# Kernel optimization log

Measured on AMD Instinct MI355X. Metric: run time of the kernel, lower is better.

The kernel has to match this reference:

```python
import jax, jax.numpy as jnp
import numpy as np

N = 40000      # nodes
E = 640000     # directed edges (avg degree 16)
IN_DIM = 64
HID = 64
OUT = 128
EPS_LN = 1e-5
EPS_BN = 1e-5
NEG_SLOPE = 0.2  # PyG GATConv default


def setup_inputs() -> dict:
    key = jax.random.key(0)
    ks = jax.random.split(key, 40)
    s = 0.05
    d = {}
    d["x"] = jax.random.normal(ks[0], (N, IN_DIM), jnp.float32)
    d["edge_index"] = jax.random.randint(ks[1], (2, E), 0, N, jnp.int32)
    d["pos"] = jax.random.normal(ks[2], (N, 3), jnp.float32)
    # GAT layer 1: in=64, out=64, heads=4 (concat)
    d["W1"] = jax.random.normal(ks[3], (4 * HID, IN_DIM), jnp.float32) * s
    d["a_s1"] = jax.random.normal(ks[4], (4, HID), jnp.float32) * s
    d["a_d1"] = jax.random.normal(ks[5], (4, HID), jnp.float32) * s
    d["bg1"] = jnp.zeros((4 * HID,), jnp.float32)
    d["ln1_g"] = jnp.ones((4 * HID,), jnp.float32)
    d["ln1_b"] = jnp.zeros((4 * HID,), jnp.float32)
    # GAT layer 2: in=256, out=64, heads=2 (concat)
    d["W2"] = jax.random.normal(ks[6], (2 * HID, 4 * HID), jnp.float32) * s
    d["a_s2"] = jax.random.normal(ks[7], (2, HID), jnp.float32) * s
    d["a_d2"] = jax.random.normal(ks[8], (2, HID), jnp.float32) * s
    d["bg2"] = jnp.zeros((2 * HID,), jnp.float32)
    d["ln2_g"] = jnp.ones((2 * HID,), jnp.float32)
    d["ln2_b"] = jnp.zeros((2 * HID,), jnp.float32)
    # GAT layer 3: in=128, out=128, heads=1
    d["W3"] = jax.random.normal(ks[9], (OUT, 2 * HID), jnp.float32) * s
    d["a_s3"] = jax.random.normal(ks[10], (1, OUT), jnp.float32) * s
    d["a_d3"] = jax.random.normal(ks[11], (1, OUT), jnp.float32) * s
    d["bg3"] = jnp.zeros((OUT,), jnp.float32)
    # pointnet: Conv1d(3,64,1) -> BN -> ReLU -> Conv1d(64,128,1) -> BN -> ReLU -> Conv1d(128,128,1)
    d["pw1"] = jax.random.normal(ks[12], (64, 3), jnp.float32) * s
    d["pb1"] = jnp.zeros((64,), jnp.float32)
    d["bn1_g"] = jnp.ones((64,), jnp.float32)
    d["bn1_b"] = jnp.zeros((64,), jnp.float32)
    d["pw2"] = jax.random.normal(ks[13], (128, 64), jnp.float32) * s
    d["pb2"] = jnp.zeros((128,), jnp.float32)
    d["bn2_g"] = jnp.ones((128,), jnp.float32)
    d["bn2_b"] = jnp.zeros((128,), jnp.float32)
    d["pw3"] = jax.random.normal(ks[14], (OUT, 128), jnp.float32) * s
    d["pb3"] = jnp.zeros((OUT,), jnp.float32)
    # fusion Linear(2*OUT, OUT)
    d["fw"] = jax.random.normal(ks[15], (OUT, 2 * OUT), jnp.float32) * s
    d["fb"] = jnp.zeros((OUT,), jnp.float32)
    return d


def _gat(x, W, a_s, a_d, b, src, dst, n):
    """PyG-style GATConv (concat=True, eval mode). x:[n,Fin], W:[H*C,Fin], a_*:[H,C]."""
    H, C = a_s.shape
    h = (x @ W.T).reshape(n, H, C)                       # [n,H,C]
    e_src = jnp.sum(h * a_s[None], -1)                   # [n,H]
    e_dst = jnp.sum(h * a_d[None], -1)                   # [n,H]
    e = jax.nn.leaky_relu(e_src[src] + e_dst[dst], NEG_SLOPE)   # [E,H]
    emax = jax.ops.segment_max(e, dst, num_segments=n)   # segment softmax over dst
    ex = jnp.exp(e - emax[dst])
    den = jax.ops.segment_sum(ex, dst, num_segments=n)
    alpha = ex / (den[dst] + 1e-16)                      # [E,H]
    out = jax.ops.segment_sum(alpha[:, :, None] * h[src], dst, num_segments=n)  # [n,H,C]
    return out.reshape(n, H * C) + b


def _ln(x, g, b):
    mu = jnp.mean(x, -1, keepdims=True)
    var = jnp.var(x, -1, keepdims=True)
    return (x - mu) * jax.lax.rsqrt(var + EPS_LN) * g + b


def _bn_eval(x, g, b):
    # eval-mode BatchNorm with freshly-initialized running stats (mean=0, var=1)
    return x * (g * jax.lax.rsqrt(jnp.float32(1.0 + EPS_BN))) + b


def reference(x, edge_index, pos, W1, a_s1, a_d1, bg1, ln1_g, ln1_b,
              W2, a_s2, a_d2, bg2, ln2_g, ln2_b, W3, a_s3, a_d3, bg3,
              pw1, pb1, bn1_g, bn1_b, pw2, pb2, bn2_g, bn2_b, pw3, pb3, fw, fb):
    n = x.shape[0]
    loops = jnp.arange(n, dtype=edge_index.dtype)        # PyG add_self_loops=True
    src = jnp.concatenate([edge_index[0], loops])
    dst = jnp.concatenate([edge_index[1], loops])

    x1 = jax.nn.relu(_ln(_gat(x, W1, a_s1, a_d1, bg1, src, dst, n), ln1_g, ln1_b))
    x2 = jax.nn.relu(_ln(_gat(x1, W2, a_s2, a_d2, bg2, src, dst, n), ln2_g, ln2_b))
    x3 = _gat(x2, W3, a_s3, a_d3, bg3, src, dst, n)      # [n,OUT]

    # pointnet: 1x1 conv1d == per-node linear
    p = jax.nn.relu(_bn_eval(pos @ pw1.T + pb1, bn1_g, bn1_b))
    p = jax.nn.relu(_bn_eval(p @ pw2.T + pb2, bn2_g, bn2_b))
    pos_features = p @ pw3.T + pb3                       # [n,OUT]

    combined = jnp.concatenate([x3, pos_features], -1)
    output = combined @ fw.T + fb
    return (output, x3, pos_features)
```

## Files before the change

### kernel.cpp

```cpp
#include <hip/hip_runtime.h>
#include <cstddef>

#define NNODES 40000
#define NEDGES 640000
#define NETOT  (NNODES + NEDGES)
#define ELLW   96
#define NCAST  30720
#define NBUCK  313
#define SEGCAP 8192
#define ABLOCKS 84
#define CBLOCKS 30
#define GBLK   625

typedef unsigned short u16;
typedef unsigned int   u32;
using v2f = __attribute__((ext_vector_type(2))) float;

__device__ inline float wave_sum(float v) {
#pragma unroll
    for (int o = 32; o > 0; o >>= 1) v += __shfl_xor(v, o);
    return v;
}
__device__ inline u16 f2bf(float f) {
    u32 u = __float_as_uint(f);
    return (u16)((u + 0x7fffu + ((u >> 16) & 1u)) >> 16);
}

__global__ void build_a_kernel(const int* __restrict__ ei, u32* __restrict__ bcnt,
                               u32* __restrict__ seg,
                               const float* __restrict__ W1, const float* __restrict__ as1,
                               const float* __restrict__ ad1, float* __restrict__ vbuf,
                               const float* s0, u16* d0, int n0, const float* s1, u16* d1, int n1,
                               const float* s2, u16* d2, int n2, const float* s3, u16* d3, int n3,
                               const float* s4, u16* d4, int n4, const float* s5, u16* d5, int n5) {
    int tid = threadIdx.x;
    int blk = blockIdx.x;
    if (blk >= ABLOCKS) {
        if (blk < ABLOCKS + CBLOCKS) {
            int i = (blk - ABLOCKS) * 1024 + tid;
            const float* s; u16* d;
            if      (i < n0) { s = s0; d = d0; }
            else if ((i -= n0) < n1) { s = s1; d = d1; }
            else if ((i -= n1) < n2) { s = s2; d = d2; }
            else if ((i -= n2) < n3) { s = s3; d = d3; }
            else if ((i -= n3) < n4) { s = s4; d = d4; }
            else if ((i -= n4) < n5) { s = s5; d = d5; }
            else return;
            float4 v = ((const float4*)s)[i];
            ushort4 o; o.x = f2bf(v.x); o.y = f2bf(v.y); o.z = f2bf(v.z); o.w = f2bf(v.w);
            ((ushort4*)d)[i] = o;
        } else if (tid < 256) {
            int h = tid >> 6, k = tid & 63;
            float ss = 0.f, dd = 0.f;
            for (int c = 0; c < 64; c++) {
                float w = W1[(h * 64 + c) * 64 + k];
                ss += as1[h * 64 + c] * w;
                dd += ad1[h * 64 + c] * w;
            }
            vbuf[tid] = ss;
            vbuf[256 + tid] = dd;
        }
        return;
    }
    __shared__ u32 hist[NBUCK], hbase[NBUCK];
    for (int i = tid; i < NBUCK; i += 1024) hist[i] = 0;
    __syncthreads();
    u32 pk[8], loc[8]; int bj[8];
    int g0 = blk * 8192;
#pragma unroll
    for (int j = 0; j < 8; j++) {
        int g = g0 + j * 1024 + tid;
        bj[j] = -1;
        if (g < NETOT) {
            int src, dst;
            if (g < NEDGES) { src = ei[g]; dst = ei[NEDGES + g]; }
            else            { src = g - NEDGES; dst = src; }
            int b = dst >> 7;
            pk[j] = ((u32)dst << 16) | (u32)src;
            bj[j] = b;
            loc[j] = atomicAdd(&hist[b], 1u);
        }
    }
    __syncthreads();
    for (int i = tid; i < NBUCK; i += 1024) {
        u32 c = hist[i];
        hbase[i] = c ? atomicAdd(&bcnt[i], c) : 0u;
    }
    __syncthreads();
#pragma unroll
    for (int j = 0; j < 8; j++) {
        if (bj[j] >= 0) {
            u32 pos = hbase[bj[j]] + loc[j];
            if (pos < SEGCAP) seg[(size_t)bj[j] * SEGCAP + pos] = pk[j];
        }
    }
}

__global__ void mid_kernel(const u32* __restrict__ seg, const u32* __restrict__ bcnt,
                           int* __restrict__ cnt, u16* __restrict__ srcs16,
                           int2* __restrict__ ovbuf,
                           const float* __restrict__ x, const float* __restrict__ vbuf,
                           float* __restrict__ es, float* __restrict__ ed, u16* __restrict__ xc,
                           const float* __restrict__ pos,
                           const float* __restrict__ pw1, const float* __restrict__ pb1,
                           const float* __restrict__ bn1g, const float* __restrict__ bn1b,
                           const u16* __restrict__ Bpn, u16* __restrict__ p2out,
                           const float* __restrict__ pb2,
                           const float* __restrict__ bn2g, const float* __restrict__ bn2b) {
    __shared__ u32 lcnt[128];
    __shared__ float vl[512];
    int tid = threadIdx.x;
    int blk = blockIdx.x;

    if (blk < NBUCK) {
        int base = blk << 7;
        if (tid < 128) lcnt[tid] = 0;
        __syncthreads();
        u32 m = bcnt[blk]; if (m > SEGCAP) m = SEGCAP;
        const u32* sp = seg + (size_t)blk * SEGCAP;
        for (u32 e = tid; e < m; e += 256) {
            u32 pkv = sp[e];
            u32 dst = pkv >> 16, src = pkv & 0xffffu;
            u32 p = atomicAdd(&lcnt[dst - (u32)base], 1u);
            if (p < ELLW) srcs16[dst * ELLW + p] = (u16)src;
            else {
                int q = atomicAdd(&cnt[NNODES], 1);
                ovbuf[q] = make_int2((int)dst, (int)src);
            }
        }
        __syncthreads();
        if (tid < 128 && base + tid < NNODES) cnt[base + tid] = (int)lcnt[tid];
        return;
    }
    blk -= NBUCK;
    if (blk < GBLK) {
        vl[tid] = vbuf[tid];
        vl[tid + 256] = vbuf[tid + 256];
        __syncthreads();
        int lane = tid & 63, wave = tid >> 6;
        int i = lane >> 2, q = lane & 3;
        int node = blk * 64 + wave * 16 + i;
        const float* xp = x + (size_t)node * 64 + q * 16;
        float xr[16];
        *(float4*)&xr[0]  = ((const float4*)xp)[0];
        *(float4*)&xr[4]  = ((const float4*)xp)[1];
        *(float4*)&xr[8]  = ((const float4*)xp)[2];
        *(float4*)&xr[12] = ((const float4*)xp)[3];
        float p[8];
#pragma unroll
        for (int h = 0; h < 8; h++) {
            float s = 0.f;
#pragma unroll
            for (int j = 0; j < 16; j++) s += xr[j] * vl[h * 64 + q * 16 + j];
            p[h] = s;
        }
#pragma unroll
        for (int h = 0; h < 8; h++) {
            p[h] += __shfl_xor(p[h], 1);
            p[h] += __shfl_xor(p[h], 2);
        }
        es[node * 4 + q] = p[q];
        ed[node * 4 + q] = p[4 + q];
        u16* cp = xc + (size_t)node * 64 + q * 16;
#pragma unroll
        for (int j = 0; j < 16; j += 4) {
            ushort4 o; o.x = f2bf(xr[j]); o.y = f2bf(xr[j + 1]);
            o.z = f2bf(xr[j + 2]); o.w = f2bf(xr[j + 3]);
            *(ushort4*)(cp + j) = o;
        }
        return;
    }
    blk -= GBLK;
    {
        const int Nn = 128, K = 64;
        using bfrag = __attribute__((ext_vector_type(8))) short;
        using ffrag = __attribute__((ext_vector_type(4))) float;
        int wave = tid >> 6, lane = tid & 63;
        int lm = lane & 15, kg = (lane >> 4) * 8;
        int rowblk = blk * 64 + wave * 16;
        int row = rowblk + lm;
        float p0 = pos[row * 3 + 0], p1 = pos[row * 3 + 1], p2 = pos[row * 3 + 2];
        const u16* Bp = Bpn + (size_t)lm * K + kg;
        const float bnscale = rsqrtf(1.0f + 1e-5f);
        ffrag acc[8] = {};
#pragma unroll
        for (int k0 = 0; k0 < K; k0 += 32) {
            bfrag af;
#pragma unroll
            for (int j = 0; j < 8; j++) {
                int k = kg + k0 + j;
                float v = p0 * pw1[k * 3 + 0] + p1 * pw1[k * 3 + 1] + p2 * pw1[k * 3 + 2] + pb1[k];
                v = v * (bn1g[k] * bnscale) + bn1b[k];
                v = v > 0.f ? v : 0.f;
                af[j] = (short)f2bf(v);
            }
#pragma unroll
            for (int t = 0; t < 8; t++) {
                bfrag bf = *(const bfrag*)(Bp + (size_t)t * 16 * K + k0);
                acc[t] = __builtin_amdgcn_mfma_f32_16x16x32_bf16(af, bf, acc[t], 0, 0, 0);
            }
        }
        int orow = rowblk + (lane >> 4) * 4;
#pragma unroll
        for (int t = 0; t < 8; t++) {
            int col = t * 16 + lm;
            float bi = pb2[col], g = bn2g[col] * bnscale, bb = bn2b[col];
#pragma unroll
            for (int r = 0; r < 4; r++) {
                float v = (acc[t][r] + bi) * g + bb;
                v = v > 0.f ? v : 0.f;
                p2out[(size_t)(orow + r) * Nn + col] = f2bf(v);
            }
        }
    }
}

__global__ void gat_agg_kernel(const u16* __restrict__ xc,
                               const float* __restrict__ es, const float* __restrict__ ed,
                               const int* __restrict__ cnt, const u16* __restrict__ srcs16,
                               const int2* __restrict__ ovbuf,
                               u16* __restrict__ agg, int n) {
    __shared__ float wbuf[4][4][100];
    __shared__ u32   sbuf[4][ELLW];
    int wave = threadIdx.x >> 6;
    int wid = (blockIdx.x * blockDim.x + threadIdx.x) >> 6;
    int lane = threadIdx.x & 63;
    if (wid >= n) return;

    int degt = cnt[wid];
    int mainc = degt < ELLW ? degt : ELLW;
    int padt = (mainc + 7) & ~7;
    const u16* sp = srcs16 + (size_t)wid * ELLW;

    const int h = lane & 3;
    const int esub = lane >> 2;
    float edh = ed[(size_t)wid * 4 + h];

    float den = 0.f;
    for (int i0 = 0; i0 < padt; i0 += 16) {
        int e = i0 + esub;
        if (e < padt) {
            float w = 0.f; u32 off = 0;
            if (e < mainc) {
                int s = sp[e];
                off = (u32)s << 7;
                float v = es[(size_t)s * 4 + h] + edh;
                v = v > 0.f ? v : 0.2f * v;
                w = __expf(v);
            }
            wbuf[wave][h][e] = w;
            if (h == 0) sbuf[wave][e] = off;
            den += w;
        }
    }
    int ovn = 0;
    if (degt > ELLW) {
        ovn = cnt[n];
        for (int j = esub; j < ovn; j += 16) {
            int2 t = ovbuf[j];
            if (t.x == wid) {
                float v = es[(size_t)t.y * 4 + h] + edh;
                v = v > 0.f ? v : 0.2f * v;
                den += __expf(v);
            }
        }
    }
#pragma unroll
    for (int o = 4; o < 64; o <<= 1) den += __shfl_xor(den, o);
    float inv = 1.f / (den + 1e-16f);

    const int e2 = lane >> 5, f16 = lane & 31;
    const char* hp = (const char*)xc + f16 * 4;
    v2f a0 = {0.f, 0.f}, a1 = {0.f, 0.f}, a2 = {0.f, 0.f}, a3 = {0.f, 0.f};
    for (int eb = 0; eb < padt; eb += 8) {
        u32 of[4]; u32 g[4];
        float w0[4], w1[4], w2[4], w3[4];
#pragma unroll
        for (int k = 0; k < 4; k++) of[k] = sbuf[wave][eb + 2 * k + e2];
#pragma unroll
        for (int k = 0; k < 4; k++) g[k] = *(const u32*)(hp + of[k]);
#pragma unroll
        for (int k = 0; k < 4; k++) {
            int e = eb + 2 * k + e2;
            w0[k] = wbuf[wave][0][e]; w1[k] = wbuf[wave][1][e];
            w2[k] = wbuf[wave][2][e]; w3[k] = wbuf[wave][3][e];
        }
#pragma unroll
        for (int k = 0; k < 4; k++) {
            v2f hx;
            hx.x = __uint_as_float(g[k] << 16);
            hx.y = __uint_as_float(g[k] & 0xffff0000u);
            a0 += v2f{w0[k], w0[k]} * hx;
            a1 += v2f{w1[k], w1[k]} * hx;
            a2 += v2f{w2[k], w2[k]} * hx;
            a3 += v2f{w3[k], w3[k]} * hx;
        }
    }
    if (degt > ELLW) {
        for (int j = 0; j < ovn; j++) {
            int2 t = ovbuf[j];
            if (t.x != wid) continue;
            float wh[4];
#pragma unroll
            for (int hh = 0; hh < 4; hh++) {
                float v = es[(size_t)t.y * 4 + hh] + __shfl(edh, hh);
                v = v > 0.f ? v : 0.2f * v;
                wh[hh] = __expf(v);
            }
            if (lane < 32) {
                u32 g = *(const u32*)(hp + ((u32)t.y << 7));
                v2f hx;
                hx.x = __uint_as_float(g << 16);
                hx.y = __uint_as_float(g & 0xffff0000u);
                a0 += v2f{wh[0], wh[0]} * hx;
                a1 += v2f{wh[1], wh[1]} * hx;
                a2 += v2f{wh[2], wh[2]} * hx;
                a3 += v2f{wh[3], wh[3]} * hx;
            }
        }
    }
    a0.x += __shfl_xor(a0.x, 32); a0.y += __shfl_xor(a0.y, 32);
    a1.x += __shfl_xor(a1.x, 32); a1.y += __shfl_xor(a1.y, 32);
    a2.x += __shfl_xor(a2.x, 32); a2.y += __shfl_xor(a2.y, 32);
    a3.x += __shfl_xor(a3.x, 32); a3.y += __shfl_xor(a3.y, 32);
    float iv[4];
#pragma unroll
    for (int hh = 0; hh < 4; hh++) iv[hh] = __shfl(inv, hh);
    if (lane < 32) {
        u32* op = (u32*)agg + (size_t)wid * 128 + f16;
        op[0]  = ((u32)f2bf(a0.y * iv[0]) << 16) | f2bf(a0.x * iv[0]);
        op[32] = ((u32)f2bf(a1.y * iv[1]) << 16) | f2bf(a1.x * iv[1]);
        op[64] = ((u32)f2bf(a2.y * iv[2]) << 16) | f2bf(a2.x * iv[2]);
        op[96] = ((u32)f2bf(a3.y * iv[3]) << 16) | f2bf(a3.x * iv[3]);
    }
}

__global__ void w1ln_kernel(const u16* __restrict__ agg, const u16* __restrict__ B,
                            const float* __restrict__ bias,
                            const float* __restrict__ lng, const float* __restrict__ lnb,
                            u16* __restrict__ xb, int M) {
    using bfrag = __attribute__((ext_vector_type(8))) short;
    using ffrag = __attribute__((ext_vector_type(4))) float;
    int wave = threadIdx.x >> 6, lane = threadIdx.x & 63;
    int lm = lane & 15, kg = (lane >> 4) * 8;
    int rowblk = blockIdx.x * 64 + wave * 16;
    ffrag acc[16] = {};
#pragma unroll
    for (int hh = 0; hh < 4; hh++) {
#pragma unroll
        for (int k0 = 0; k0 < 64; k0 += 32) {
            bfrag af = *(const bfrag*)(agg + (size_t)(rowblk + lm) * 256 + hh * 64 + kg + k0);
#pragma unroll
            for (int tt = 0; tt < 4; tt++) {
                int t = hh * 4 + tt;
                bfrag bf = *(const bfrag*)(B + (size_t)(hh * 64 + tt * 16 + lm) * 64 + kg + k0);
                acc[t] = __builtin_amdgcn_mfma_f32_16x16x32_bf16(af, bf, acc[t], 0, 0, 0);
            }
        }
    }
    int orow = rowblk + (lane >> 4) * 4;
    float bi[16], gg[16], bb[16];
#pragma unroll
    for (int t = 0; t < 16; t++) {
        int col = t * 16 + lm;
        bi[t] = bias[col]; gg[t] = lng[col]; bb[t] = lnb[col];
    }
#pragma unroll
    for (int r = 0; r < 4; r++) {
        float pv[16];
        float s1 = 0.f, s2 = 0.f;
#pragma unroll
        for (int t = 0; t < 16; t++) {
            float v = acc[t][r] + bi[t];
            pv[t] = v; s1 += v; s2 += v * v;
        }
#pragma unroll
        for (int o = 1; o < 16; o <<= 1) { s1 += __shfl_xor(s1, o); s2 += __shfl_xor(s2, o); }
        float mu = s1 / 256.f;
        float var = s2 / 256.f - mu * mu;
        float rstd = rsqrtf(var + 1e-5f);
#pragma unroll
        for (int t = 0; t < 16; t++) {
            float v = (pv[t] - mu) * rstd * gg[t] + bb[t];
            v = v > 0.f ? v : 0.f;
            xb[(size_t)(orow + r) * 256 + t * 16 + lm] = f2bf(v);
        }
    }
}

template <int H, int C, bool AF32>
__global__ void gemm_scores_kernel(const void* __restrict__ Aptr, const u16* __restrict__ B,
                                   u16* __restrict__ Cout,
                                   const float* __restrict__ as, const float* __restrict__ ad,
                                   float* __restrict__ es, float* __restrict__ ed,
                                   int M, int Nn, int K) {
    constexpr int HT = 128 / C;
    using bfrag = __attribute__((ext_vector_type(8))) short;
    using ffrag = __attribute__((ext_vector_type(4))) float;
    int wave = threadIdx.x >> 6, lane = threadIdx.x & 63;
    int lm = lane & 15, kg = (lane >> 4) * 8;
    int rowblk = blockIdx.x * 64 + wave * 16;
    int n0 = blockIdx.y * 128;
    const u16* Bp = B + (size_t)(n0 + lm) * K + kg;
    ffrag acc[8] = {};
    for (int k0 = 0; k0 < K; k0 += 32) {
        bfrag af;
        if constexpr (AF32) {
            const float* ap = (const float*)Aptr + (size_t)(rowblk + lm) * K + kg + k0;
            float4 a0 = *(const float4*)ap;
            float4 a1 = *(const float4*)(ap + 4);
            af[0] = (short)f2bf(a0.x); af[1] = (short)f2bf(a0.y);
            af[2] = (short)f2bf(a0.z); af[3] = (short)f2bf(a0.w);
            af[4] = (short)f2bf(a1.x); af[5] = (short)f2bf(a1.y);
            af[6] = (short)f2bf(a1.z); af[7] = (short)f2bf(a1.w);
        } else {
            af = *(const bfrag*)((const u16*)Aptr + (size_t)(rowblk + lm) * K + kg + k0);
        }
#pragma unroll
        for (int t = 0; t < 8; t++) {
            bfrag bf = *(const bfrag*)(Bp + (size_t)t * 16 * K + k0);
            acc[t] = __builtin_amdgcn_mfma_f32_16x16x32_bf16(af, bf, acc[t], 0, 0, 0);
        }
    }
    int orow = rowblk + (lane >> 4) * 4;
    float asv[8], adv[8];
#pragma unroll
    for (int t = 0; t < 8; t++) {
        int fcol = n0 + t * 16 + lm;
        asv[t] = as[fcol]; adv[t] = ad[fcol];
    }
    float ps[4][HT] = {}, pd[4][HT] = {};
#pragma unroll
    for (int t = 0; t < 8; t++) {
        const int hh = t / (C / 16);
#pragma unroll
        for (int r = 0; r < 4; r++) {
            float v = acc[t][r];
            ps[r][hh] += v * asv[t];
            pd[r][hh] += v * adv[t];
            Cout[(size_t)(orow + r) * Nn + n0 + t * 16 + lm] = f2bf(v);
        }
    }
    int hb = blockIdx.y * HT;
#pragma unroll
    for (int r = 0; r < 4; r++)
#pragma unroll
        for (int hh = 0; hh < HT; hh++) {
            float s = ps[r][hh], d = pd[r][hh];
#pragma unroll
            for (int o = 1; o < 16; o <<= 1) { s += __shfl_xor(s, o); d += __shfl_xor(d, o); }
            if (lm == 0) {
                es[(size_t)(orow + r) * H + hb + hh] = s;
                ed[(size_t)(orow + r) * H + hb + hh] = d;
            }
        }
}

template <int H, int C, bool LNRELU>
__global__ void gat_fused_kernel(const u16* __restrict__ hmat,
                                 const float* __restrict__ es, const float* __restrict__ ed,
                                 const int* __restrict__ cnt, const u16* __restrict__ srcs16,
                                 const int2* __restrict__ ovbuf,
                                 const float* __restrict__ bias,
                                 const float* __restrict__ lng, const float* __restrict__ lnb,
                                 void* __restrict__ out, u16* __restrict__ x16out, int n) {
    constexpr int HC = H * C;
    constexpr int VPT = HC / 64;
    constexpr int SH = (HC == 256) ? 9 : 8;
    constexpr int EPW = 64 / H;
    constexpr int HSH = (H == 4) ? 2 : ((H == 2) ? 1 : 0);
    __shared__ float wbuf[4][H][100];
    __shared__ int   sbuf[4][ELLW];
    int wave = threadIdx.x >> 6;
    int wid = (blockIdx.x * blockDim.x + threadIdx.x) >> 6;
    int lane = threadIdx.x & 63;
    if (wid >= n) return;

    int degt = cnt[wid];
    int mainc = degt < ELLW ? degt : ELLW;
    int pad = (mainc + 7) & ~7;
    const u16* sp = srcs16 + (size_t)wid * ELLW;

    const int h = lane & (H - 1);
    const int esub = lane >> HSH;
    float edh = ed[(size_t)wid * H + h];

    float den = 0.f;
    for (int i0 = 0; i0 < pad; i0 += EPW) {
        int e = i0 + esub;
        if (e < pad) {
            float w = 0.f;
            int soff = 0;
            if (e < mainc) {
                int s = sp[e];
                soff = s << SH;
                float v = es[(size_t)s * H + h] + edh;
                v = v > 0.f ? v : 0.2f * v;
                w = __expf(v);
            }
            wbuf[wave][h][e] = w;
            if (h == 0) sbuf[wave][e] = soff;
            den += w;
        }
    }
    int ovn = 0;
    if (degt > ELLW) {
        ovn = cnt[n];
        for (int j = esub; j < ovn; j += EPW) {
            int2 t = ovbuf[j];
            if (t.x == wid) {
                float v = es[(size_t)t.y * H + h] + edh;
                v = v > 0.f ? v : 0.2f * v;
                den += __expf(v);
            }
        }
    }
#pragma unroll
    for (int o = H; o < 64; o <<= 1) den += __shfl_xor(den, o);
    float inv = 1.f / (den + 1e-16f);

    const int myhead = (lane * VPT) / C;
    const float invh = __shfl(inv, myhead);
    const int loff = lane * (VPT * 2);
    v2f a01 = {0.f, 0.f}, a23 = {0.f, 0.f};

    for (int e = 0; e < pad; e += 8) {
        int4   o0 = *(const int4*)&sbuf[wave][e];
        int4   o1 = *(const int4*)&sbuf[wave][e + 4];
        float4 w0 = *(const float4*)&wbuf[wave][myhead][e];
        float4 w1 = *(const float4*)&wbuf[wave][myhead][e + 4];
        int   oo[8] = {o0.x, o0.y, o0.z, o0.w, o1.x, o1.y, o1.z, o1.w};
        float ww[8] = {w0.x, w0.y, w0.z, w0.w, w1.x, w1.y, w1.z, w1.w};
        if constexpr (VPT == 4) {
            uint2 gg[8];
#pragma unroll
            for (int u = 0; u < 8; u++)
                gg[u] = *(const uint2*)((const char*)hmat + (size_t)(u32)oo[u] + loff);
#pragma unroll
            for (int u = 0; u < 8; u++) {
                v2f wv = {ww[u], ww[u]};
                v2f h01, h23;
                h01.x = __uint_as_float(gg[u].x << 16);
                h01.y = __uint_as_float(gg[u].x & 0xffff0000u);
                h23.x = __uint_as_float(gg[u].y << 16);
                h23.y = __uint_as_float(gg[u].y & 0xffff0000u);
                a01 += wv * h01;
                a23 += wv * h23;
            }
        } else {
            u32 gg[8];
#pragma unroll
            for (int u = 0; u < 8; u++)
                gg[u] = *(const u32*)((const char*)hmat + (size_t)(u32)oo[u] + loff);
#pragma unroll
            for (int u = 0; u < 8; u++) {
                v2f wv = {ww[u], ww[u]};
                v2f h01;
                h01.x = __uint_as_float(gg[u] << 16);
                h01.y = __uint_as_float(gg[u] & 0xffff0000u);
                a01 += wv * h01;
            }
        }
    }
    if (degt > ELLW) {
        const float edm = __shfl(edh, myhead);
        for (int j = 0; j < ovn; j++) {
            int2 t = ovbuf[j];
            if (t.x != wid) continue;
            float v = es[(size_t)t.y * H + myhead] + edm;
            v = v > 0.f ? v : 0.2f * v;
            float w = __expf(v);
            v2f wv = {w, w};
            if constexpr (VPT == 4) {
                uint2 g = *(const uint2*)((const char*)hmat + ((size_t)t.y << SH) + loff);
                v2f h01, h23;
                h01.x = __uint_as_float(g.x << 16);
                h01.y = __uint_as_float(g.x & 0xffff0000u);
                h23.x = __uint_as_float(g.y << 16);
                h23.y = __uint_as_float(g.y & 0xffff0000u);
                a01 += wv * h01;
                a23 += wv * h23;
            } else {
                u32 g = *(const u32*)((const char*)hmat + ((size_t)t.y << SH) + loff);
                v2f h01;
                h01.x = __uint_as_float(g << 16);
                h01.y = __uint_as_float(g & 0xffff0000u);
                a01 += wv * h01;
            }
        }
    }
    {
        v2f iv = {invh, invh};
        a01 *= iv;
        a23 *= iv;
    }

    int fbase = lane * VPT;
    float y[VPT];
    y[0] = a01.x + bias[fbase + 0];
    y[1] = a01.y + bias[fbase + 1];
    if constexpr (VPT == 4) {
        y[2] = a23.x + bias[fbase + 2];
        y[3] = a23.y + bias[fbase + 3];
    }

    if constexpr (LNRELU) {
        float s1 = 0.f, s2 = 0.f;
#pragma unroll
        for (int j = 0; j < VPT; j++) { s1 += y[j]; s2 += y[j] * y[j]; }
        s1 = wave_sum(s1);
        s2 = wave_sum(s2);
        float mu = s1 / (float)HC;
        float var = s2 / (float)HC - mu * mu;
        float rstd = rsqrtf(var + 1e-5f);
#pragma unroll
        for (int j = 0; j < VPT; j++) {
            float v = (y[j] - mu) * rstd * lng[fbase + j] + lnb[fbase + j];
            y[j] = v > 0.f ? v : 0.f;
        }
        u16* op = (u16*)out + (size_t)wid * HC + fbase;
        if constexpr (VPT == 4) {
            ushort4 o; o.x = f2bf(y[0]); o.y = f2bf(y[1]); o.z = f2bf(y[2]); o.w = f2bf(y[3]);
            *(ushort4*)op = o;
        } else {
            ushort2 o; o.x = f2bf(y[0]); o.y = f2bf(y[1]);
            *(ushort2*)op = o;
        }
    } else {
        float* op = (float*)out + (size_t)wid * HC + fbase;
        if constexpr (VPT == 4) *(float4*)op = make_float4(y[0], y[1], y[2], y[3]);
        else                    *(float2*)op = make_float2(y[0], y[1]);
        if (x16out) {
            if constexpr (VPT == 4) {
                ushort4 o; o.x = f2bf(y[0]); o.y = f2bf(y[1]); o.z = f2bf(y[2]); o.w = f2bf(y[3]);
                *(ushort4*)&x16out[(size_t)wid * HC + fbase] = o;
            } else {
                ushort2 o; o.x = f2bf(y[0]); o.y = f2bf(y[1]);
                *(ushort2*)&x16out[(size_t)wid * HC + fbase] = o;
            }
        }
    }
}

__global__ void gemm_pw3cat_kernel(const u16* __restrict__ p2, const u16* __restrict__ Bpw3,
                                   const float* __restrict__ pb3, float* __restrict__ pf,
                                   const u16* __restrict__ x3b, const u16* __restrict__ Bfw,
                                   const float* __restrict__ fb, float* __restrict__ outp,
                                   int M) {
    using bfrag = __attribute__((ext_vector_type(8))) short;
    using ffrag = __attribute__((ext_vector_type(4))) float;
    __shared__ float pft[64][132];
    int wave = threadIdx.x >> 6, lane = threadIdx.x & 63;
    int lm = lane & 15, kg = (lane >> 4) * 8;
    int rowblk = blockIdx.x * 64 + wave * 16;
    int rowbase = blockIdx.x * 64;
    int row = rowblk + lm;

    bfrag afg[4];
#pragma unroll
    for (int i = 0; i < 4; i++)
        afg[i] = *(const bfrag*)(x3b + (size_t)row * 128 + kg + i * 32);

    {
        bfrag afs[4];
#pragma unroll
        for (int i = 0; i < 4; i++)
            afs[i] = *(const bfrag*)(p2 + (size_t)row * 128 + kg + i * 32);
        const u16* Bp = Bpw3 + (size_t)lm * 128 + kg;
        ffrag acc[8] = {};
#pragma unroll
        for (int k = 0; k < 4; k++)
#pragma unroll
            for (int t = 0; t < 8; t++) {
                bfrag bf = *(const bfrag*)(Bp + (size_t)t * 16 * 128 + k * 32);
                acc[t] = __builtin_amdgcn_mfma_f32_16x16x32_bf16(afs[k], bf, acc[t], 0, 0, 0);
            }
        int lrow = wave * 16 + (lane >> 4) * 4;
#pragma unroll
        for (int t = 0; t < 8; t++) {
            int col = t * 16 + lm;
            float bi = pb3[col];
#pragma unroll
            for (int r = 0; r < 4; r++)
                pft[lrow + r][col] = acc[t][r] + bi;
        }
    }
    __syncthreads();

    for (int i = threadIdx.x; i < 2048; i += 256) {
        int rw = i >> 5, c4 = (i & 31) << 2;
        float4 v = *(const float4*)&pft[rw][c4];
        *(float4*)&pf[(size_t)(rowbase + rw) * 128 + c4] = v;
    }

    {
        int lrow = wave * 16 + lm;
        bfrag afl[4];
#pragma unroll
        for (int i = 0; i < 4; i++) {
            const float* ap = &pft[lrow][kg + i * 32];
            float4 a0 = *(const float4*)ap;
            float4 a1 = *(const float4*)(ap + 4);
            bfrag af;
            af[0] = (short)f2bf(a0.x); af[1] = (short)f2bf(a0.y);
            af[2] = (short)f2bf(a0.z); af[3] = (short)f2bf(a0.w);
            af[4] = (short)f2bf(a1.x); af[5] = (short)f2bf(a1.y);
            af[6] = (short)f2bf(a1.z); af[7] = (short)f2bf(a1.w);
            afl[i] = af;
        }
        const u16* Bp = Bfw + (size_t)lm * 256 + kg;
        ffrag acc[8] = {};
#pragma unroll
        for (int k = 0; k < 8; k++) {
            bfrag af = (k < 4) ? afg[k] : afl[k - 4];
#pragma unroll
            for (int t = 0; t < 8; t++) {
                bfrag bf = *(const bfrag*)(Bp + (size_t)t * 16 * 256 + k * 32);
                acc[t] = __builtin_amdgcn_mfma_f32_16x16x32_bf16(af, bf, acc[t], 0, 0, 0);
            }
        }
        __syncthreads();
        int lrow2 = wave * 16 + (lane >> 4) * 4;
#pragma unroll
        for (int t = 0; t < 8; t++) {
            int col = t * 16 + lm;
            float bi = fb[col];
#pragma unroll
            for (int r = 0; r < 4; r++)
                pft[lrow2 + r][col] = acc[t][r] + bi;
        }
        __syncthreads();
        for (int i = threadIdx.x; i < 2048; i += 256) {
            int rw2 = i >> 5, c4 = (i & 31) << 2;
            float4 v = *(const float4*)&pft[rw2][c4];
            *(float4*)&outp[(size_t)(rowbase + rw2) * 128 + c4] = v;
        }
    }
}

extern "C" void kernel_launch(void* const* d_in, const int* in_sizes, int n_in,
                              void* d_out, int out_size, void* d_ws, size_t ws_size,
                              hipStream_t stream) {
    const float* x    = (const float*)d_in[0];
    const int*   ei   = (const int*)d_in[1];
    const float* pos  = (const float*)d_in[2];
    const float* W1   = (const float*)d_in[3];
    const float* as1  = (const float*)d_in[4];
    const float* ad1  = (const float*)d_in[5];
    const float* bg1  = (const float*)d_in[6];
    const float* ln1g = (const float*)d_in[7];
    const float* ln1b = (const float*)d_in[8];
    const float* W2   = (const float*)d_in[9];
    const float* as2  = (const float*)d_in[10];
    const float* ad2  = (const float*)d_in[11];
    const float* bg2  = (const float*)d_in[12];
    const float* ln2g = (const float*)d_in[13];
    const float* ln2b = (const float*)d_in[14];
    const float* W3   = (const float*)d_in[15];
    const float* as3  = (const float*)d_in[16];
    const float* ad3  = (const float*)d_in[17];
    const float* bg3  = (const float*)d_in[18];
    const float* pw1  = (const float*)d_in[19];
    const float* pb1  = (const float*)d_in[20];
    const float* bn1g = (const float*)d_in[21];
    const float* bn1b = (const float*)d_in[22];
    const float* pw2  = (const float*)d_in[23];
    const float* pb2  = (const float*)d_in[24];
    const float* bn2g = (const float*)d_in[25];
    const float* bn2b = (const float*)d_in[26];
    const float* pw3  = (const float*)d_in[27];
    const float* pb3  = (const float*)d_in[28];
    const float* fw   = (const float*)d_in[29];
    const float* fb   = (const float*)d_in[30];

    const int N = NNODES;
    float* out = (float*)d_out;
    float* x3  = out + (size_t)N * 128;
    float* pf  = out + (size_t)2 * N * 128;

    char* ws = (char*)d_ws;
    size_t off = 0;
    auto alloc = [&](size_t bytes) -> void* {
        void* p = ws + off;
        off += (bytes + 255) / 256 * 256;
        return p;
    };
    int*   cnt    = (int*)alloc((size_t)(N + 1 + NBUCK) * 4);
    u32*   bcnt   = (u32*)(cnt + N + 1);
    u32*   seg    = (u32*)alloc((size_t)NBUCK * SEGCAP * 4);
    u16*   srcs16 = (u16*)alloc((size_t)N * ELLW * 2);
    int2*  ovbuf  = (int2*)alloc((size_t)NETOT * 8);
    float* esb    = (float*)alloc((size_t)N * 4 * 4);
    float* edb    = (float*)alloc((size_t)N * 4 * 4);
    u16*   w1c    = (u16*)alloc(16384 * 2);
    u16*   w2c    = (u16*)alloc(32768 * 2);
    u16*   w3c    = (u16*)alloc(16384 * 2);
    u16*   pw2c   = (u16*)alloc(8192 * 2);
    u16*   pw3c   = (u16*)alloc(16384 * 2);
    u16*   fwc    = (u16*)alloc(32768 * 2);
    u16*   hbufb  = (u16*)alloc((size_t)N * 128 * 2);
    u16*   xb     = (u16*)alloc((size_t)N * 256 * 2);
    u16*   p2b    = (u16*)alloc((size_t)N * 128 * 2);
    u16*   xc     = (u16*)alloc((size_t)N * 64 * 2);
    float* vbuf   = (float*)alloc(512 * 4);
    u16*   aggb   = (u16*)alloc((size_t)N * 256 * 2);
    u16*   x3b    = (u16*)alloc((size_t)N * 128 * 2);

    hipMemsetAsync(cnt, 0, (size_t)(N + 1 + NBUCK) * 4, stream);
    build_a_kernel<<<ABLOCKS + CBLOCKS + 1, 1024, 0, stream>>>(
        ei, bcnt, seg, W1, as1, ad1, vbuf,
        W1, w1c, 4096, W2, w2c, 8192, W3, w3c, 4096,
        pw2, pw2c, 2048, pw3, pw3c, 4096, fw, fwc, 8192);

    mid_kernel<<<NBUCK + 2 * GBLK, 256, 0, stream>>>(
        seg, bcnt, cnt, srcs16, ovbuf,
        x, vbuf, esb, edb, xc,
        pos, pw1, pb1, bn1g, bn1b, pw2c, p2b, pb2, bn2g, bn2b);

    const int NW = N / 4;
    const int GB = GBLK;

    gat_agg_kernel<<<NW, 256, 0, stream>>>(xc, esb, edb, cnt, srcs16, ovbuf, aggb, N);
    w1ln_kernel<<<GB, 256, 0, stream>>>(aggb, w1c, bg1, ln1g, ln1b, xb, N);

    gemm_scores_kernel<2, 64, false><<<dim3(GB, 1), 256, 0, stream>>>(
        xb, w2c, hbufb, as2, ad2, esb, edb, N, 128, 256);
    gat_fused_kernel<2, 64, true><<<NW, 256, 0, stream>>>(
        hbufb, esb, edb, cnt, srcs16, ovbuf, bg2, ln2g, ln2b, xb, nullptr, N);

    gemm_scores_kernel<1, 128, false><<<dim3(GB, 1), 256, 0, stream>>>(
        xb, w3c, hbufb, as3, ad3, esb, edb, N, 128, 128);
    gat_fused_kernel<1, 128, false><<<NW, 256, 0, stream>>>(
        hbufb, esb, edb, cnt, srcs16, ovbuf, bg3, nullptr, nullptr, x3, x3b, N);

    gemm_pw3cat_kernel<<<GB, 256, 0, stream>>>(p2b, pw3c, pb3, pf, x3b, fwc, fb, out, N);
}
```

Before: 352.2 us.

## Split final fused GEMM into two LDS-staged kernels and batch B-fragment loads

```diff
diff --git a/kernel.cpp b/kernel.cpp
--- a/kernel.cpp
+++ b/kernel.cpp
@@ -335,7 +335,8 @@
     }
 }
 
-__global__ void w1ln_kernel(const u16* __restrict__ agg, const u16* __restrict__ B,
+__global__ __launch_bounds__(256, 2) void w1ln_kernel(
+                            const u16* __restrict__ agg, const u16* __restrict__ B,
                             const float* __restrict__ bias,
                             const float* __restrict__ lng, const float* __restrict__ lnb,
                             u16* __restrict__ xb, int M) {
@@ -350,11 +351,14 @@
 #pragma unroll
         for (int k0 = 0; k0 < 64; k0 += 32) {
             bfrag af = *(const bfrag*)(agg + (size_t)(rowblk + lm) * 256 + hh * 64 + kg + k0);
+            bfrag bfs[4];
+#pragma unroll
+            for (int tt = 0; tt < 4; tt++)
+                bfs[tt] = *(const bfrag*)(B + (size_t)(hh * 64 + tt * 16 + lm) * 64 + kg + k0);
 #pragma unroll
             for (int tt = 0; tt < 4; tt++) {
                 int t = hh * 4 + tt;
-                bfrag bf = *(const bfrag*)(B + (size_t)(hh * 64 + tt * 16 + lm) * 64 + kg + k0);
-                acc[t] = __builtin_amdgcn_mfma_f32_16x16x32_bf16(af, bf, acc[t], 0, 0, 0);
+                acc[t] = __builtin_amdgcn_mfma_f32_16x16x32_bf16(af, bfs[tt], acc[t], 0, 0, 0);
             }
         }
     }
@@ -389,7 +393,8 @@
 }
 
 template <int H, int C, bool AF32>
-__global__ void gemm_scores_kernel(const void* __restrict__ Aptr, const u16* __restrict__ B,
+__global__ __launch_bounds__(256, 2) void gemm_scores_kernel(
+                                   const void* __restrict__ Aptr, const u16* __restrict__ B,
                                    u16* __restrict__ Cout,
                                    const float* __restrict__ as, const float* __restrict__ ad,
                                    float* __restrict__ es, float* __restrict__ ed,
@@ -416,11 +421,13 @@
         } else {
             af = *(const bfrag*)((const u16*)Aptr + (size_t)(rowblk + lm) * K + kg + k0);
         }
-#pragma unroll
-        for (int t = 0; t < 8; t++) {
-            bfrag bf = *(const bfrag*)(Bp + (size_t)t * 16 * K + k0);
-            acc[t] = __builtin_amdgcn_mfma_f32_16x16x32_bf16(af, bf, acc[t], 0, 0, 0);
-        }
+        bfrag bfs[8];
+#pragma unroll
+        for (int t = 0; t < 8; t++)
+            bfs[t] = *(const bfrag*)(Bp + (size_t)t * 16 * K + k0);
+#pragma unroll
+        for (int t = 0; t < 8; t++)
+            acc[t] = __builtin_amdgcn_mfma_f32_16x16x32_bf16(af, bfs[t], acc[t], 0, 0, 0);
     }
     int orow = rowblk + (lane >> 4) * 4;
     float asv[8], adv[8];
@@ -642,99 +649,85 @@
     }
 }
 
-__global__ void gemm_pw3cat_kernel(const u16* __restrict__ p2, const u16* __restrict__ Bpw3,
-                                   const float* __restrict__ pb3, float* __restrict__ pf,
-                                   const u16* __restrict__ x3b, const u16* __restrict__ Bfw,
-                                   const float* __restrict__ fb, float* __restrict__ outp,
-                                   int M) {
+__global__ void pf_kernel(const u16* __restrict__ p2, const u16* __restrict__ Bpw3,
+                          const float* __restrict__ pb3, float* __restrict__ pf,
+                          u16* __restrict__ pfb, int M) {
     using bfrag = __attribute__((ext_vector_type(8))) short;
     using ffrag = __attribute__((ext_vector_type(4))) float;
-    __shared__ float pft[64][132];
-    int wave = threadIdx.x >> 6, lane = threadIdx.x & 63;
+    __shared__ u16 bl[128][136];
+    int tid = threadIdx.x;
+    for (int i = tid; i < 2048; i += 256) {
+        int r = i >> 4, c = (i & 15) * 8;
+        *(uint4*)&bl[r][c] = *(const uint4*)(Bpw3 + (size_t)r * 128 + c);
+    }
+    __syncthreads();
+    int wave = tid >> 6, lane = tid & 63;
     int lm = lane & 15, kg = (lane >> 4) * 8;
-    int rowblk = blockIdx.x * 64 + wave * 16;
-    int rowbase = blockIdx.x * 64;
-    int row = rowblk + lm;
-
-    bfrag afg[4];
+    int row = blockIdx.x * 64 + wave * 16 + lm;
+    bfrag afs[4];
 #pragma unroll
     for (int i = 0; i < 4; i++)
-        afg[i] = *(const bfrag*)(x3b + (size_t)row * 128 + kg + i * 32);
-
-    {
-        bfrag afs[4];
-#pragma unroll
-        for (int i = 0; i < 4; i++)
-            afs[i] = *(const bfrag*)(p2 + (size_t)row * 128 + kg + i * 32);
-        const u16* Bp = Bpw3 + (size_t)lm * 128 + kg;
-        ffrag acc[8] = {};
-#pragma unroll
-        for (int k = 0; k < 4; k++)
-#pragma unroll
-            for (int t = 0; t < 8; t++) {
-                bfrag bf = *(const bfrag*)(Bp + (size_t)t * 16 * 128 + k * 32);
-                acc[t] = __builtin_amdgcn_mfma_f32_16x16x32_bf16(afs[k], bf, acc[t], 0, 0, 0);
-            }
-        int lrow = wave * 16 + (lane >> 4) * 4;
+        afs[i] = *(const bfrag*)(p2 + (size_t)row * 128 + kg + i * 32);
+    ffrag acc[8] = {};
+#pragma unroll
+    for (int k = 0; k < 4; k++)
 #pragma unroll
         for (int t = 0; t < 8; t++) {
-            int col = t * 16 + lm;
-            float bi = pb3[col];
-#pragma unroll
-            for (int r = 0; r < 4; r++)
-                pft[lrow + r][col] = acc[t][r] + bi;
-        }
+            bfrag bf = *(const bfrag*)&bl[t * 16 + lm][kg + k * 32];
+            acc[t] = __builtin_amdgcn_mfma_f32_16x16x32_bf16(afs[k], bf, acc[t], 0, 0, 0);
+        }
+    int orow = blockIdx.x * 64 + wave * 16 + (lane >> 4) * 4;
+#pragma unroll
+    for (int t = 0; t < 8; t++) {
+        int col = t * 16 + lm;
+        float bi = pb3[col];
+#pragma unroll
+        for (int r = 0; r < 4; r++) {
+            float v = acc[t][r] + bi;
+            pf[(size_t)(orow + r) * 128 + col] = v;
+            pfb[(size_t)(orow + r) * 128 + col] = f2bf(v);
+        }
+    }
+}
+
+__global__ void out_kernel(const u16* __restrict__ x3b, const u16* __restrict__ pfb,
+                           const u16* __restrict__ Bfw, const float* __restrict__ fb,
+                           float* __restrict__ outp, int M) {
+    using bfrag = __attribute__((ext_vector_type(8))) short;
+    using ffrag = __attribute__((ext_vector_type(4))) float;
+    __shared__ u16 bl[128][264];
+    int tid = threadIdx.x;
+    for (int i = tid; i < 4096; i += 256) {
+        int r = i >> 5, c = (i & 31) * 8;
+        *(uint4*)&bl[r][c] = *(const uint4*)(Bfw + (size_t)r * 256 + c);
     }
     __syncthreads();
-
-    for (int i = threadIdx.x; i < 2048; i += 256) {
-        int rw = i >> 5, c4 = (i & 31) << 2;
-        float4 v = *(const float4*)&pft[rw][c4];
-        *(float4*)&pf[(size_t)(rowbase + rw) * 128 + c4] = v;
-    }
-
-    {
-        int lrow = wave * 16 + lm;
-        bfrag afl[4];
-#pragma unroll
-        for (int i = 0; i < 4; i++) {
-            const float* ap = &pft[lrow][kg + i * 32];
-            float4 a0 = *(const float4*)ap;
-            float4 a1 = *(const float4*)(ap + 4);
-            bfrag af;
-            af[0] = (short)f2bf(a0.x); af[1] = (short)f2bf(a0.y);
-            af[2] = (short)f2bf(a0.z); af[3] = (short)f2bf(a0.w);
-            af[4] = (short)f2bf(a1.x); af[5] = (short)f2bf(a1.y);
-            af[6] = (short)f2bf(a1.z); af[7] = (short)f2bf(a1.w);
-            afl[i] = af;
-        }
-        const u16* Bp = Bfw + (size_t)lm * 256 + kg;
-        ffrag acc[8] = {};
-#pragma unroll
-        for (int k = 0; k < 8; k++) {
-            bfrag af = (k < 4) ? afg[k] : afl[k - 4];
-#pragma unroll
-            for (int t = 0; t < 8; t++) {
-                bfrag bf = *(const bfrag*)(Bp + (size_t)t * 16 * 256 + k * 32);
-                acc[t] = __builtin_amdgcn_mfma_f32_16x16x32_bf16(af, bf, acc[t], 0, 0, 0);
-            }
-        }
-        __syncthreads();
-        int lrow2 = wave * 16 + (lane >> 4) * 4;
+    int wave = tid >> 6, lane = tid & 63;
+    int lm = lane & 15, kg = (lane >> 4) * 8;
+    int row = blockIdx.x * 64 + wave * 16 + lm;
+    bfrag afs[8];
+#pragma unroll
+    for (int i = 0; i < 4; i++)
+        afs[i] = *(const bfrag*)(x3b + (size_t)row * 128 + kg + i * 32);
+#pragma unroll
+    for (int i = 0; i < 4; i++)
+        afs[4 + i] = *(const bfrag*)(pfb + (size_t)row * 128 + kg + i * 32);
+    ffrag acc[8] = {};
+#pragma unroll
+    for (int k = 0; k < 8; k++)
 #pragma unroll
         for (int t = 0; t < 8; t++) {
-            int col = t * 16 + lm;
-            float bi = fb[col];
-#pragma unroll
-            for (int r = 0; r < 4; r++)
-                pft[lrow2 + r][col] = acc[t][r] + bi;
-        }
-        __syncthreads();
-        for (int i = threadIdx.x; i < 2048; i += 256) {
-            int rw2 = i >> 5, c4 = (i & 31) << 2;
-            float4 v = *(const float4*)&pft[rw2][c4];
-            *(float4*)&outp[(size_t)(rowbase + rw2) * 128 + c4] = v;
-        }
+            bfrag bf = *(const bfrag*)&bl[t * 16 + lm][kg + k * 32];
+            acc[t] = __builtin_amdgcn_mfma_f32_16x16x32_bf16(afs[k], bf, acc[t], 0, 0, 0);
+        }
+    int orow = blockIdx.x * 64 + wave * 16 + (lane >> 4) * 4;
+#pragma unroll
+    for (int t = 0; t < 8; t++) {
+        int col = t * 16 + lm;
+        float bi = fb[col];
+#pragma unroll
+        for (int r = 0; r < 4; r++)
+            outp[(size_t)(orow + r) * 128 + col] = acc[t][r] + bi;
     }
 }
 
@@ -805,6 +798,7 @@
     float* vbuf   = (float*)alloc(512 * 4);
     u16*   aggb   = (u16*)alloc((size_t)N * 256 * 2);
     u16*   x3b    = (u16*)alloc((size_t)N * 128 * 2);
+    u16*   pfb    = (u16*)alloc((size_t)N * 128 * 2);
 
     hipMemsetAsync(cnt, 0, (size_t)(N + 1 + NBUCK) * 4, stream);
     build_a_kernel<<<ABLOCKS + CBLOCKS + 1, 1024, 0, stream>>>(
@@ -833,5 +827,6 @@
     gat_fused_kernel<1, 128, false><<<NW, 256, 0, stream>>>(
         hbufb, esb, edb, cnt, srcs16, ovbuf, bg3, nullptr, nullptr, x3, x3b, N);
 
-    gemm_pw3cat_kernel<<<GB, 256, 0, stream>>>(p2b, pw3c, pb3, pf, x3b, fwc, fb, out, N);
-}
+    pf_kernel<<<GB, 256, 0, stream>>>(p2b, pw3c, pb3, pf, pfb, N);
+    out_kernel<<<GB, 256, 0, stream>>>(x3b, pfb, fwc, fb, out, N);
+}
```

Result: faster. 334.8 us (-4.9%).
